# Performance work log

Measured on AMD Instinct MI355X. Metric: run time of the kernel, lower is better.

The kernel has to match this reference:

```python
import jax, jax.numpy as jnp
import numpy as np

B, S, I, H, O, L = 32, 512, 1024, 1024, 1024, 2
W_SCALE = 0.03  # keep gate pre-activations in a sane range


def setup_inputs() -> dict:
    key = jax.random.key(0)
    ks = jax.random.split(key, 10)
    rn = lambda k, shape: jax.random.normal(k, shape, dtype=jnp.float32)
    return {
        "x": rn(ks[0], (B, S, I)),
        "h0": jnp.zeros((L, B, H), jnp.float32),
        "Wxz": rn(ks[1], (L, H, H)) * W_SCALE,
        "Wxr": rn(ks[2], (L, H, H)) * W_SCALE,
        "Wxg": rn(ks[3], (L, H, H)) * W_SCALE,
        "Whz": rn(ks[4], (L, H, H)) * W_SCALE,
        "Whr": rn(ks[5], (L, H, H)) * W_SCALE,
        "Whg": rn(ks[6], (L, H, H)) * W_SCALE,
        "bhz": jnp.zeros((L, H), jnp.float32),
        "bhr": jnp.zeros((L, H), jnp.float32),
        "bhg": jnp.zeros((L, H), jnp.float32),
        "WY": rn(ks[7], (O, H)) * W_SCALE,
        "bY": jnp.zeros((O,), jnp.float32),
    }


def reference(x, h0, Wxz, Wxr, Wxg, Whz, Whr, Whg, bhz, bhr, bhg, WY, bY):
    # x: [B,S,I]; h0: [L,B,H]. PyTorch Linear: y = x @ W.T (+ b).
    def step(h, x_t):            # h: [L,B,H], x_t: [B,I]
        xk = x_t
        new_h = []
        for k in range(L):       # static small layer loop
            hk = h[k]
            z = jax.nn.sigmoid(xk @ Wxz[k].T + hk @ Whz[k].T + bhz[k])
            r = jax.nn.sigmoid(xk @ Wxr[k].T + hk @ Whr[k].T + bhr[k])
            g = jnp.tanh(xk @ Wxg[k].T + (r * hk) @ Whg[k].T + bhg[k])
            hk = z * hk + (1.0 - z) * g
            new_h.append(hk)
            xk = hk              # dropout=0 -> identity
        y_t = xk @ WY.T + bY     # [B,O]
        return jnp.stack(new_h), y_t

    h_final, ys = jax.lax.scan(step, h0, jnp.swapaxes(x, 0, 1))  # ys: [S,B,O]
    layer_output = jnp.swapaxes(ys, 0, 1)                         # [B,S,O]
    hidden_state = jnp.swapaxes(h_final, 0, 1)                    # [B,L,H]
    return layer_output, hidden_state
```

## Files before the change

### kernel.cpp

```cpp
#include <hip/hip_runtime.h>
#include <hip/hip_bf16.h>

typedef __bf16 bf16x8 __attribute__((ext_vector_type(8)));
typedef float floatx4 __attribute__((ext_vector_type(4)));

#define HID 1024
#define HH (1024*1024)
#define SEQ 512
#define NB 32768
#define NBLK 256

__device__ __forceinline__ float bf2f(unsigned short u) {
  union { unsigned int i; float f; } v; v.i = ((unsigned int)u) << 16; return v.f;
}
__device__ __forceinline__ unsigned short f2bf(float f) {
  union { float f; unsigned int i; } v; v.f = f;
  unsigned int i = v.i;
  return (unsigned short)((i + 0x7fffu + ((i >> 16) & 1u)) >> 16);
}
__device__ __forceinline__ float ldflag(const void* p, long i, int flag) {
  return flag ? ((const float*)p)[i] : bf2f(((const unsigned short*)p)[i]);
}
__device__ __forceinline__ float sigmoidf_(float x) { return 1.0f / (1.0f + __expf(-x)); }

#define GSTH(p_, v_)   asm volatile("global_store_short %0, %1, off sc0 sc1" :: "v"(p_), "v"(v_) : "memory")
#define GSTW(p_, v_)   asm volatile("global_store_dword %0, %1, off sc0 sc1" :: "v"(p_), "v"(v_) : "memory")

__device__ __forceinline__ void outw_wt(void* out, int flag, long idx, float v) {
  if (flag) { GSTW((float*)out + idx, v); }
  else      { GSTH((unsigned short*)out + idx, (unsigned int)f2bf(v)); }
}

__global__ void detect_k(const unsigned int* __restrict__ xw, int* __restrict__ flag) {
  unsigned int w = xw[threadIdx.x];
  int e = (w >> 7) & 0xFF;
  int ok = (e >= 100 && e <= 141) ? 1 : 0;
  unsigned long long m = __ballot(ok);
  if (threadIdx.x == 0) *flag = (__popcll(m) >= 36) ? 0 : 1;
}

__global__ void convert_k(const float* __restrict__ x,
                          const float* __restrict__ w0, const float* __restrict__ w1,
                          const float* __restrict__ w2, const float* __restrict__ w3,
                          const float* __restrict__ w4, const float* __restrict__ w5,
                          const float* __restrict__ wy,
                          unsigned short* __restrict__ xb, unsigned short* __restrict__ wc,
                          unsigned short* __restrict__ wyc, const int* __restrict__ flag) {
  if (*flag == 0) return;
  const float* Ws[6] = { w0, w1, w2, w3, w4, w5 };
  const long total = 3801088;
  for (long c = (long)blockIdx.x * 256 + threadIdx.x; c < total; c += (long)gridDim.x * 256) {
    long e = c * 8;
    const float* src; unsigned short* dst; long off;
    if (e < 16777216)      { src = x;  dst = xb;  off = e; }
    else if (e < 29360128) { long r = e - 16777216; int wi = (int)(r >> 21);
                             src = Ws[wi]; dst = wc + (long)wi * 2097152; off = r & 2097151; }
    else                   { src = wy; dst = wyc; off = e - 29360128; }
    float4 a = *(const float4*)(src + off);
    float4 b = *(const float4*)(src + off + 4);
    uint4 o;
    o.x = (unsigned)f2bf(a.x) | ((unsigned)f2bf(a.y) << 16);
    o.y = (unsigned)f2bf(a.z) | ((unsigned)f2bf(a.w) << 16);
    o.z = (unsigned)f2bf(b.x) | ((unsigned)f2bf(b.y) << 16);
    o.w = (unsigned)f2bf(b.z) | ((unsigned)f2bf(b.w) << 16);
    *(uint4*)(dst + off) = o;
  }
}

__device__ __forceinline__ void gbar(int* cnt, int target, int blk) {
  __syncthreads();
  if (threadIdx.x == 0) {
    __builtin_amdgcn_fence(__ATOMIC_RELEASE, "agent");
    __hip_atomic_fetch_add(cnt + (blk & 7) * 64, 1, __ATOMIC_RELAXED, __HIP_MEMORY_SCOPE_AGENT);
    int ssum;
    do {
      ssum = 0;
      #pragma unroll
      for (int i = 0; i < 8; ++i)
        ssum += __hip_atomic_load(cnt + i * 64, __ATOMIC_RELAXED, __HIP_MEMORY_SCOPE_AGENT);
      if (ssum < target) __builtin_amdgcn_s_sleep(1);
    } while (ssum < target);
    __builtin_amdgcn_fence(__ATOMIC_ACQUIRE, "agent");
  }
  __syncthreads();
}

__device__ __forceinline__ void gbar2(int* xcdArr, int* gCnt, int* xcdTick, int* xcdGo,
                                      int myxcd, int xcdTot, int pidx) {
  asm volatile("s_waitcnt vmcnt(0)" ::: "memory");
  __syncthreads();
  if (threadIdx.x == 0) {
    int old = __hip_atomic_fetch_add(xcdArr + myxcd * 64, 1,
                                     __ATOMIC_RELAXED, __HIP_MEMORY_SCOPE_AGENT);
    if (old == pidx * xcdTot - 1) {
      __builtin_amdgcn_fence(__ATOMIC_RELEASE, "agent");
      __hip_atomic_fetch_add(gCnt + myxcd * 64, xcdTot,
                             __ATOMIC_RELAXED, __HIP_MEMORY_SCOPE_AGENT);
    }
    const int target = NBLK * pidx;
    int ssum;
    do {
      ssum = 0;
      #pragma unroll
      for (int i = 0; i < 8; ++i)
        ssum += __hip_atomic_load(gCnt + i * 64, __ATOMIC_RELAXED, __HIP_MEMORY_SCOPE_AGENT);
      if (ssum < target) __builtin_amdgcn_s_sleep(1);
    } while (ssum < target);
    int t = __hip_atomic_fetch_add(xcdTick + myxcd * 64, 1,
                                   __ATOMIC_RELAXED, __HIP_MEMORY_SCOPE_AGENT);
    if (t == (pidx - 1) * xcdTot) {
      __builtin_amdgcn_fence(__ATOMIC_ACQUIRE, "agent");
      asm volatile("s_waitcnt vmcnt(0)" ::: "memory");
      __hip_atomic_store(xcdGo + myxcd * 64, pidx,
                         __ATOMIC_RELAXED, __HIP_MEMORY_SCOPE_AGENT);
    } else {
      while (__hip_atomic_load(xcdGo + myxcd * 64, __ATOMIC_RELAXED,
                               __HIP_MEMORY_SCOPE_AGENT) < pidx)
        __builtin_amdgcn_s_sleep(1);
      asm volatile("buffer_inv" ::: "memory");
    }
  }
  __syncthreads();
}

__device__ __forceinline__ void stage2(unsigned short* dst,
                                       const unsigned short* __restrict__ s0,
                                       const unsigned short* __restrict__ s1,
                                       int n0, int tid) {
  const unsigned short* srcs[2] = { s0, s1 };
  #pragma unroll
  for (int i = 0; i < 16; ++i) {
    int idx = i * 256 + tid;
    int m = idx >> 11;
    int rem = idx & 2047;
    int r = rem >> 7, k8 = rem & 127;
    bf16x8 v = *(const bf16x8*)(srcs[m] + (long)(n0 + r) * HID + k8 * 8);
    int kc = k8 >> 2, L = ((k8 & 3) << 4) | r;
    *(bf16x8*)(dst + (((m * 32 + kc) * 64 + L) << 3)) = v;
  }
}
__device__ __forceinline__ void stage1(unsigned short* dst,
                                       const unsigned short* __restrict__ s0,
                                       int n0, int tid) {
  #pragma unroll
  for (int i = 0; i < 8; ++i) {
    int idx = i * 256 + tid;
    int r = idx >> 7, k8 = idx & 127;
    bf16x8 v = *(const bf16x8*)(s0 + (long)(n0 + r) * HID + k8 * 8);
    int kc = k8 >> 2, L = ((k8 & 3) << 4) | r;
    *(bf16x8*)(dst + ((kc * 64 + L) << 3)) = v;
  }
}

__device__ __forceinline__ floatx4 gpair(const unsigned short* __restrict__ a1,
                                         const unsigned short* __restrict__ a2,
                                         const unsigned short* sW, int khalf, int lane) {
  floatx4 acc = {0.f, 0.f, 0.f, 0.f};
  const unsigned short* w1 = sW + (((khalf * 16) * 64 + lane) << 3);
  const unsigned short* w2 = sW + (((32 + khalf * 16) * 64 + lane) << 3);
  #pragma unroll
  for (int j = 0; j < 16; ++j)
    acc = __builtin_amdgcn_mfma_f32_16x16x32_bf16(*(const bf16x8*)(a1 + j * 32),
                                                  *(const bf16x8*)(w1 + j * 512), acc, 0, 0, 0);
  #pragma unroll
  for (int j = 0; j < 16; ++j)
    acc = __builtin_amdgcn_mfma_f32_16x16x32_bf16(*(const bf16x8*)(a2 + j * 32),
                                                  *(const bf16x8*)(w2 + j * 512), acc, 0, 0, 0);
  return acc;
}
__device__ __forceinline__ floatx4 gsingle(const unsigned short* __restrict__ a,
                                           const unsigned short* sW, int khalf, int lane) {
  floatx4 acc = {0.f, 0.f, 0.f, 0.f};
  const unsigned short* w = sW + (((khalf * 16) * 64 + lane) << 3);
  #pragma unroll
  for (int j = 0; j < 16; ++j)
    acc = __builtin_amdgcn_mfma_f32_16x16x32_bf16(*(const bf16x8*)(a + j * 32),
                                                  *(const bf16x8*)(w + j * 512), acc, 0, 0, 0);
  return acc;
}

__global__ void __launch_bounds__(256, 1) gru2(
    const void* __restrict__ x, const void* __restrict__ h0i,
    const void* __restrict__ Wxz, const void* __restrict__ Wxr, const void* __restrict__ Wxg,
    const void* __restrict__ Whz, const void* __restrict__ Whr, const void* __restrict__ Whg,
    const void* __restrict__ bhz, const void* __restrict__ bhr, const void* __restrict__ bhg,
    const void* __restrict__ WY, const void* __restrict__ bY,
    void* __restrict__ out, const int* __restrict__ flagp, int* __restrict__ barBase,
    const unsigned short* __restrict__ xb, const unsigned short* __restrict__ wcv,
    const unsigned short* __restrict__ wyc,
    float* __restrict__ h0f, float* __restrict__ h1f,
    float* __restrict__ z0f, float* __restrict__ z1f,
    unsigned short* __restrict__ h0b, unsigned short* __restrict__ h1b,
    unsigned short* __restrict__ rh0, unsigned short* __restrict__ rh1)
{
  extern __shared__ char smem[];
  unsigned short* sWP = (unsigned short*)smem;
  unsigned short* sWQ = (unsigned short*)(smem + 65536);
  floatx4* red = (floatx4*)(smem + 131072);

  int* barCnt   = barBase;
  int* xcdArr   = barBase + 512;
  int* gCnt     = barBase + 1024;
  int* xcdTick  = barBase + 1536;
  int* xcdGo    = barBase + 2048;
  int* xcdCount = barBase + 2560;

  const int flag = *flagp;
  const int thr  = threadIdx.x;
  const int wave = thr >> 6;
  const int lane = thr & 63;
  const int l15  = lane & 15;
  const int kq   = (lane >> 4) * 8;
  const int blk  = blockIdx.x;
  const int role = blk >> 6;
  const int c0   = (blk & 63) * 16;
  const int myxcd = __builtin_amdgcn_s_getreg(20 | (3 << 11)) & 7;

  const unsigned short* xP  = flag ? xb                : (const unsigned short*)x;
  const unsigned short* Wzp = flag ? wcv + 0L*2097152  : (const unsigned short*)Wxz;
  const unsigned short* Wrp = flag ? wcv + 1L*2097152  : (const unsigned short*)Wxr;
  const unsigned short* Wgp = flag ? wcv + 2L*2097152  : (const unsigned short*)Wxg;
  const unsigned short* Uzp = flag ? wcv + 3L*2097152  : (const unsigned short*)Whz;
  const unsigned short* Urp = flag ? wcv + 4L*2097152  : (const unsigned short*)Whr;
  const unsigned short* Ugp = flag ? wcv + 5L*2097152  : (const unsigned short*)Whg;
  const unsigned short* WYp = flag ? wyc               : (const unsigned short*)WY;

  if (thr == 0)
    __hip_atomic_fetch_add(xcdCount + myxcd * 64, 1, __ATOMIC_RELAXED, __HIP_MEMORY_SCOPE_AGENT);

  {
    long off = (role >> 1) ? (long)HH : 0;
    const unsigned short* s0 = ((role & 1) ? Wrp : Wzp) + off;
    const unsigned short* s1 = ((role & 1) ? Urp : Uzp) + off;
    stage2(sWP, s0, s1, c0, thr);
  }
  if (blk < 128)      stage2(sWQ, Wgp + (blk >= 64 ? (long)HH : 0),
                             Ugp + (blk >= 64 ? (long)HH : 0), c0, thr);
  else if (blk < 192) stage1(sWQ, WYp, (blk - 128) * 16, thr);

  {
    int gtid = blk * 256 + thr;
    int layer = gtid >> 15, i = gtid & 32767;
    float v = ldflag(h0i, (long)layer * NB + i, flag);
    unsigned int b = f2bf(v);
    if (layer == 0) { GSTW(h0f + i, v); GSTH(h0b + i, b); GSTH(h0b + NB + i, b); }
    else            { GSTW(h1f + i, v); GSTH(h1b + i, b); GSTH(h1b + NB + i, b); }
  }
  asm volatile("s_waitcnt vmcnt(0)" ::: "memory");
  gbar(barCnt, NBLK, blk);

  int xcdTot = 0;
  if (thr == 0)
    xcdTot = __hip_atomic_load(xcdCount + myxcd * 64, __ATOMIC_RELAXED, __HIP_MEMORY_SCOPE_AGENT);
  int pidx = 0;

  for (int s = 0; s < SEQ + 2; ++s) {
    const int pPrev  = ((s + 1) & 1) * NB;
    const int pPrev2 = (s & 1) * NB;
    const int mt = wave & 1, khalf = wave >> 1;
    const int m = mt * 16 + l15;
    const int aoff = kq + khalf * 512;

    {
      const int layer = role >> 1, zr = role & 1;
      const bool active = layer ? (s >= 1 && s <= SEQ) : (s < SEQ);
      if (active) {
        const unsigned short *a1, *a2;
        if (layer == 0) {
          a1 = xP + (long)m * (SEQ * HID) + (long)s * HID + aoff;
          a2 = h0b + pPrev + m * HID + aoff;
        } else {
          a1 = h0b + pPrev + m * HID + aoff;
          a2 = h1b + pPrev2 + m * HID + aoff;
        }
        floatx4 acc = gpair(a1, a2, sWP, khalf, lane);
        red[wave * 64 + lane] = acc;
        __syncthreads();
        if (wave < 2) {
          floatx4 ss = red[wave * 64 + lane] + red[(wave + 2) * 64 + lane];
          int n = c0 + l15;
          float bv = ldflag(zr ? bhr : bhz, (long)layer * HID + n, flag);
          #pragma unroll
          for (int r = 0; r < 4; ++r) {
            int row = wave * 16 + (lane >> 4) * 4 + r;
            int idx = row * HID + n;
            float v = sigmoidf_(ss[r] + bv);
            if (role == 0)      GSTW(z0f + idx, v);
            else if (role == 1) GSTH(rh0 + idx, (unsigned int)f2bf(v * h0f[idx]));
            else if (role == 2) GSTW(z1f + idx, v);
            else                GSTH(rh1 + idx, (unsigned int)f2bf(v * h1f[idx]));
          }
        }
      }
    }
    ++pidx; gbar2(xcdArr, gCnt, xcdTick, xcdGo, myxcd, xcdTot, pidx);

    if (role == 0) {
      if (s < SEQ) {
        const unsigned short* a1 = xP + (long)m * (SEQ * HID) + (long)s * HID + aoff;
        const unsigned short* a2 = rh0 + m * HID + aoff;
        floatx4 acc = gpair(a1, a2, sWQ, khalf, lane);
        red[wave * 64 + lane] = acc;
        __syncthreads();
        if (wave < 2) {
          floatx4 ss = red[wave * 64 + lane] + red[(wave + 2) * 64 + lane];
          int n = c0 + l15;
          float bv = ldflag(bhg, n, flag);
          #pragma unroll
          for (int r = 0; r < 4; ++r) {
            int row = wave * 16 + (lane >> 4) * 4 + r;
            int idx = row * HID + n;
            float g = tanhf(ss[r] + bv);
            float z = z0f[idx], hp = h0f[idx];
            float hn = z * hp + (1.f - z) * g;
            GSTW(h0f + idx, hn);
            GSTH(h0b + (s & 1) * NB + idx, (unsigned int)f2bf(hn));
            if (s == SEQ - 1) outw_wt(out, flag, 16777216L + (long)row * 2048 + n, hn);
          }
        }
      }
    } else if (role == 1) {
      if (s >= 1 && s <= SEQ) {
        const unsigned short* a1 = h0b + pPrev + m * HID + aoff;
        const unsigned short* a2 = rh1 + m * HID + aoff;
        floatx4 acc = gpair(a1, a2, sWQ, khalf, lane);
        red[wave * 64 + lane] = acc;
        __syncthreads();
        if (wave < 2) {
          floatx4 ss = red[wave * 64 + lane] + red[(wave + 2) * 64 + lane];
          int n = c0 + l15;
          float bv = ldflag(bhg, (long)HID + n, flag);
          #pragma unroll
          for (int r = 0; r < 4; ++r) {
            int row = wave * 16 + (lane >> 4) * 4 + r;
            int idx = row * HID + n;
            float g = tanhf(ss[r] + bv);
            float z = z1f[idx], hp = h1f[idx];
            float hn = z * hp + (1.f - z) * g;
            GSTW(h1f + idx, hn);
            GSTH(h1b + ((s + 1) & 1) * NB + idx, (unsigned int)f2bf(hn));
            if (s == SEQ) outw_wt(out, flag, 16777216L + (long)row * 2048 + 1024 + n, hn);
          }
        }
      }
    } else if (role == 2) {
      if (s >= 2) {
        const int cy = (blk - 128) * 16;
        const unsigned short* a = h1b + pPrev2 + m * HID + aoff;
        floatx4 acc = gsingle(a, sWQ, khalf, lane);
        red[wave * 64 + lane] = acc;
        __syncthreads();
        if (wave < 2) {
          floatx4 ss = red[wave * 64 + lane] + red[(wave + 2) * 64 + lane];
          int n = cy + l15;
          float bv = ldflag(bY, n, flag);
          const int tY = s - 2;
          #pragma unroll
          for (int r = 0; r < 4; ++r) {
            int brow = wave * 16 + (lane >> 4) * 4 + r;
            long oidx = ((long)brow * SEQ + tY) * HID + n;
            outw_wt(out, flag, oidx, ss[r] + bv);
          }
        }
      }
    }
    ++pidx; gbar2(xcdArr, gCnt, xcdTick, xcdGo, myxcd, xcdTot, pidx);
  }
}

extern "C" void kernel_launch(void* const* d_in, const int* in_sizes, int n_in,
                              void* d_out, int out_size, void* d_ws, size_t ws_size,
                              hipStream_t stream) {
  const void* x   = d_in[0];
  const void* h0i = d_in[1];
  const void* Wxz = d_in[2];
  const void* Wxr = d_in[3];
  const void* Wxg = d_in[4];
  const void* Whz = d_in[5];
  const void* Whr = d_in[6];
  const void* Whg = d_in[7];
  const void* bhz = d_in[8];
  const void* bhr = d_in[9];
  const void* bhg = d_in[10];
  const void* WY  = d_in[11];
  const void* bY  = d_in[12];

  char* ws = (char*)d_ws;
  int* flag    = (int*)ws;
  int* barBase = (int*)(ws + 1024);
  float* h0f = (float*)(ws + 16384);
  float* h1f = h0f + NB;
  float* z0f = h1f + NB;
  float* z1f = z0f + NB;
  unsigned short* h0b = (unsigned short*)(z1f + NB);
  unsigned short* h1b = h0b + 2 * NB;
  unsigned short* rh0 = h1b + 2 * NB;
  unsigned short* rh1 = rh0 + NB;
  unsigned short* xb  = (unsigned short*)(ws + (1 << 20));
  unsigned short* wcv = xb + 16777216L;
  unsigned short* wyc = wcv + 12582912L;

  hipMemsetAsync(barBase, 0, 12288, stream);
  detect_k<<<1, 64, 0, stream>>>((const unsigned int*)x, flag);
  convert_k<<<2048, 256, 0, stream>>>((const float*)x,
      (const float*)Wxz, (const float*)Wxr, (const float*)Wxg,
      (const float*)Whz, (const float*)Whr, (const float*)Whg,
      (const float*)WY, xb, wcv, wyc, flag);

  static int attr_set = 0;
  if (!attr_set) {
    hipFuncSetAttribute((const void*)gru2, hipFuncAttributeMaxDynamicSharedMemorySize, 135168);
    attr_set = 1;
  }

  void* out = d_out;
  const int* flagc = flag;
  int* barc = barBase;
  void* args[] = { (void*)&x, (void*)&h0i, (void*)&Wxz, (void*)&Wxr, (void*)&Wxg,
                   (void*)&Whz, (void*)&Whr, (void*)&Whg, (void*)&bhz, (void*)&bhr,
                   (void*)&bhg, (void*)&WY, (void*)&bY, (void*)&out, (void*)&flagc,
                   (void*)&barc, (void*)&xb, (void*)&wcv, (void*)&wyc,
                   (void*)&h0f, (void*)&h1f, (void*)&z0f, (void*)&z1f,
                   (void*)&h0b, (void*)&h1b, (void*)&rh0, (void*)&rh1 };
  hipLaunchCooperativeKernel((const void*)gru2, dim3(NBLK), dim3(256), args, 135168, stream);
}
```

Measured before the change: 8.760 ms.

## Use per-XCD leader barrier and paired atomic-exchange stores for cross-block state

```diff
diff --git a/kernel.cpp b/kernel.cpp
--- a/kernel.cpp
+++ b/kernel.cpp
@@ -26,9 +26,14 @@
 #define GSTH(p_, v_)   asm volatile("global_store_short %0, %1, off sc0 sc1" :: "v"(p_), "v"(v_) : "memory")
 #define GSTW(p_, v_)   asm volatile("global_store_dword %0, %1, off sc0 sc1" :: "v"(p_), "v"(v_) : "memory")
 
-__device__ __forceinline__ void outw_wt(void* out, int flag, long idx, float v) {
-  if (flag) { GSTW((float*)out + idx, v); }
-  else      { GSTH((unsigned short*)out + idx, (unsigned int)f2bf(v)); }
+__device__ __forceinline__ void aswapF2(float* addr, float lo, float hi) {
+  union { float f[2]; unsigned long long u; } p; p.f[0] = lo; p.f[1] = hi;
+  __hip_atomic_exchange((unsigned long long*)addr, p.u,
+                        __ATOMIC_RELAXED, __HIP_MEMORY_SCOPE_AGENT);
+}
+__device__ __forceinline__ void aswapH2(unsigned short* addr, unsigned lo, unsigned hi) {
+  __hip_atomic_exchange((unsigned int*)addr, (lo & 0xffffu) | (hi << 16),
+                        __ATOMIC_RELAXED, __HIP_MEMORY_SCOPE_AGENT);
 }
 
 __global__ void detect_k(const unsigned int* __restrict__ xw, int* __restrict__ flag) {
@@ -85,32 +90,27 @@
   __syncthreads();
 }
 
-__device__ __forceinline__ void gbar2(int* xcdArr, int* gCnt, int* xcdTick, int* xcdGo,
-                                      int myxcd, int xcdTot, int pidx) {
+__device__ __forceinline__ void gbar3(int* xcdArr, int* gCnt, int* xcdGo,
+                                      int myxcd, int xcdTot, int lead, int pidx) {
   asm volatile("s_waitcnt vmcnt(0)" ::: "memory");
   __syncthreads();
   if (threadIdx.x == 0) {
-    int old = __hip_atomic_fetch_add(xcdArr + myxcd * 64, 1,
-                                     __ATOMIC_RELAXED, __HIP_MEMORY_SCOPE_AGENT);
-    if (old == pidx * xcdTot - 1) {
-      __builtin_amdgcn_fence(__ATOMIC_RELEASE, "agent");
+    __hip_atomic_fetch_add(xcdArr + myxcd * 64, 1, __ATOMIC_RELAXED, __HIP_MEMORY_SCOPE_AGENT);
+    if (lead) {
+      while (__hip_atomic_load(xcdArr + myxcd * 64, __ATOMIC_RELAXED,
+                               __HIP_MEMORY_SCOPE_AGENT) < pidx * xcdTot)
+        __builtin_amdgcn_s_sleep(1);
       __hip_atomic_fetch_add(gCnt + myxcd * 64, xcdTot,
                              __ATOMIC_RELAXED, __HIP_MEMORY_SCOPE_AGENT);
-    }
-    const int target = NBLK * pidx;
-    int ssum;
-    do {
-      ssum = 0;
-      #pragma unroll
-      for (int i = 0; i < 8; ++i)
-        ssum += __hip_atomic_load(gCnt + i * 64, __ATOMIC_RELAXED, __HIP_MEMORY_SCOPE_AGENT);
-      if (ssum < target) __builtin_amdgcn_s_sleep(1);
-    } while (ssum < target);
-    int t = __hip_atomic_fetch_add(xcdTick + myxcd * 64, 1,
-                                   __ATOMIC_RELAXED, __HIP_MEMORY_SCOPE_AGENT);
-    if (t == (pidx - 1) * xcdTot) {
+      int ssum;
+      do {
+        ssum = 0;
+        #pragma unroll
+        for (int i = 0; i < 8; ++i)
+          ssum += __hip_atomic_load(gCnt + i * 64, __ATOMIC_RELAXED, __HIP_MEMORY_SCOPE_AGENT);
+        if (ssum < NBLK * pidx) __builtin_amdgcn_s_sleep(1);
+      } while (ssum < NBLK * pidx);
       __builtin_amdgcn_fence(__ATOMIC_ACQUIRE, "agent");
-      asm volatile("s_waitcnt vmcnt(0)" ::: "memory");
       __hip_atomic_store(xcdGo + myxcd * 64, pidx,
                          __ATOMIC_RELAXED, __HIP_MEMORY_SCOPE_AGENT);
     } else {
@@ -201,7 +201,6 @@
   int* barCnt   = barBase;
   int* xcdArr   = barBase + 512;
   int* gCnt     = barBase + 1024;
-  int* xcdTick  = barBase + 1536;
   int* xcdGo    = barBase + 2048;
   int* xcdCount = barBase + 2560;
 
@@ -214,6 +213,7 @@
   const int blk  = blockIdx.x;
   const int role = blk >> 6;
   const int c0   = (blk & 63) * 16;
+  const bool evn = (lane & 1) == 0;
   const int myxcd = __builtin_amdgcn_s_getreg(20 | (3 << 11)) & 7;
 
   const unsigned short* xP  = flag ? xb                : (const unsigned short*)x;
@@ -225,8 +225,12 @@
   const unsigned short* Ugp = flag ? wcv + 5L*2097152  : (const unsigned short*)Whg;
   const unsigned short* WYp = flag ? wyc               : (const unsigned short*)WY;
 
-  if (thr == 0)
-    __hip_atomic_fetch_add(xcdCount + myxcd * 64, 1, __ATOMIC_RELAXED, __HIP_MEMORY_SCOPE_AGENT);
+  int lead = 0;
+  if (thr == 0) {
+    int old = __hip_atomic_fetch_add(xcdCount + myxcd * 64, 1,
+                                     __ATOMIC_RELAXED, __HIP_MEMORY_SCOPE_AGENT);
+    lead = (old == 0);
+  }
 
   {
     long off = (role >> 1) ? (long)HH : 0;
@@ -280,20 +284,31 @@
           floatx4 ss = red[wave * 64 + lane] + red[(wave + 2) * 64 + lane];
           int n = c0 + l15;
           float bv = ldflag(zr ? bhr : bhz, (long)layer * HID + n, flag);
-          #pragma unroll
-          for (int r = 0; r < 4; ++r) {
-            int row = wave * 16 + (lane >> 4) * 4 + r;
-            int idx = row * HID + n;
-            float v = sigmoidf_(ss[r] + bv);
-            if (role == 0)      GSTW(z0f + idx, v);
-            else if (role == 1) GSTH(rh0 + idx, (unsigned int)f2bf(v * h0f[idx]));
-            else if (role == 2) GSTW(z1f + idx, v);
-            else                GSTH(rh1 + idx, (unsigned int)f2bf(v * h1f[idx]));
+          if (!zr) {
+            float* zdst = layer ? z1f : z0f;
+            #pragma unroll
+            for (int r = 0; r < 4; ++r) {
+              int row = wave * 16 + (lane >> 4) * 4 + r;
+              float v = sigmoidf_(ss[r] + bv);
+              float vp = __shfl_xor(v, 1);
+              if (evn) aswapF2(zdst + row * HID + n, v, vp);
+            }
+          } else {
+            const float* hsrc = layer ? h1f : h0f;
+            unsigned short* rdst = layer ? rh1 : rh0;
+            #pragma unroll
+            for (int r = 0; r < 4; ++r) {
+              int row = wave * 16 + (lane >> 4) * 4 + r;
+              int idx = row * HID + n;
+              unsigned sv = f2bf(sigmoidf_(ss[r] + bv) * hsrc[idx]);
+              unsigned pv = __shfl_xor((int)sv, 1);
+              if (evn) aswapH2(rdst + idx, sv, pv);
+            }
           }
         }
       }
     }
-    ++pidx; gbar2(xcdArr, gCnt, xcdTick, xcdGo, myxcd, xcdTot, pidx);
+    ++pidx; gbar3(xcdArr, gCnt, xcdGo, myxcd, xcdTot, lead, pidx);
 
     if (role == 0) {
       if (s < SEQ) {
@@ -313,9 +328,18 @@
             float g = tanhf(ss[r] + bv);
             float z = z0f[idx], hp = h0f[idx];
             float hn = z * hp + (1.f - z) * g;
-            GSTW(h0f + idx, hn);
-            GSTH(h0b + (s & 1) * NB + idx, (unsigned int)f2bf(hn));
-            if (s == SEQ - 1) outw_wt(out, flag, 16777216L + (long)row * 2048 + n, hn);
+            float hnp = __shfl_xor(hn, 1);
+            unsigned hb = f2bf(hn);
+            unsigned hbp = __shfl_xor((int)hb, 1);
+            if (evn) {
+              aswapF2(h0f + idx, hn, hnp);
+              aswapH2(h0b + (s & 1) * NB + idx, hb, hbp);
+              if (s == SEQ - 1) {
+                long o = 16777216L + (long)row * 2048 + n;
+                if (flag) aswapF2((float*)out + o, hn, hnp);
+                else      aswapH2((unsigned short*)out + o, hb, hbp);
+              }
+            }
           }
         }
       }
@@ -337,9 +361,18 @@
             float g = tanhf(ss[r] + bv);
             float z = z1f[idx], hp = h1f[idx];
             float hn = z * hp + (1.f - z) * g;
-            GSTW(h1f + idx, hn);
-            GSTH(h1b + ((s + 1) & 1) * NB + idx, (unsigned int)f2bf(hn));
-            if (s == SEQ) outw_wt(out, flag, 16777216L + (long)row * 2048 + 1024 + n, hn);
+            float hnp = __shfl_xor(hn, 1);
+            unsigned hb = f2bf(hn);
+            unsigned hbp = __shfl_xor((int)hb, 1);
+            if (evn) {
+              aswapF2(h1f + idx, hn, hnp);
+              aswapH2(h1b + ((s + 1) & 1) * NB + idx, hb, hbp);
+              if (s == SEQ) {
+                long o = 16777216L + (long)row * 2048 + 1024 + n;
+                if (flag) aswapF2((float*)out + o, hn, hnp);
+                else      aswapH2((unsigned short*)out + o, hb, hbp);
+              }
+            }
           }
         }
       }
@@ -359,12 +392,19 @@
           for (int r = 0; r < 4; ++r) {
             int brow = wave * 16 + (lane >> 4) * 4 + r;
             long oidx = ((long)brow * SEQ + tY) * HID + n;
-            outw_wt(out, flag, oidx, ss[r] + bv);
+            float yv = ss[r] + bv;
+            float yp = __shfl_xor(yv, 1);
+            unsigned yb = f2bf(yv);
+            unsigned ybp = __shfl_xor((int)yb, 1);
+            if (evn) {
+              if (flag) aswapF2((float*)out + oidx, yv, yp);
+              else      aswapH2((unsigned short*)out + oidx, yb, ybp);
+            }
           }
         }
       }
     }
-    ++pidx; gbar2(xcdArr, gCnt, xcdTick, xcdGo, myxcd, xcdTot, pidx);
+    ++pidx; gbar3(xcdArr, gCnt, xcdGo, myxcd, xcdTot, lead, pidx);
   }
 }
 
```

After: 10.71 ms. +22.3%, slower.
